# Kernel optimization log

Measured on AMD Instinct MI355X. Metric: run time of the kernel, lower is better.

The kernel has to match this reference:

```python
import jax, jax.numpy as jnp
import numpy as np

WS = 8          # window size
SS = WS // 2    # shift size
HEADS = 16
DIM = 512
H = W = 256
L = WS * WS


def _rel_pos_index(ws):
    coords = np.stack(np.meshgrid(np.arange(ws), np.arange(ws), indexing='ij')).reshape(2, -1)
    rel = coords[:, :, None] - coords[:, None, :]            # (2, L, L)
    return (rel[0] + ws - 1) * (2 * ws - 1) + (rel[1] + ws - 1)  # (L, L)


def _shift_mask(H, W, ws, ss):
    m = np.zeros((H, W), np.int32)
    cnt = 0
    for hs in (slice(0, -ws), slice(-ws, -ss), slice(-ss, None)):
        for wsl in (slice(0, -ws), slice(-ws, -ss), slice(-ss, None)):
            m[hs, wsl] = cnt
            cnt += 1
    m = m.reshape(H // ws, ws, W // ws, ws).transpose(0, 2, 1, 3).reshape(-1, ws * ws)
    return m[:, None, :] != m[:, :, None]  # (num_windows, L, L) bool


REL_IDX = jnp.asarray(_rel_pos_index(WS))          # (L, L) int32
MASK = jnp.asarray(_shift_mask(H, W, WS, SS))      # (nw, L, L) bool


def setup_inputs() -> dict:
    key = jax.random.key(0)
    ks = jax.random.split(key, 16)
    d = DIM
    s = lambda *sh: 1.0 / np.sqrt(sh[0])
    return {
        'x': jax.random.normal(ks[0], (1, d, H, W), jnp.float32),
        'norm1_w': jnp.ones((d,), jnp.float32),
        'norm1_b': jnp.zeros((d,), jnp.float32),
        'qkv_w': jax.random.normal(ks[1], (d, 3 * d), jnp.float32) * s(d),
        'qkv_b': jnp.zeros((3 * d,), jnp.float32),
        'proj_w': jax.random.normal(ks[2], (d, d), jnp.float32) * s(d),
        'proj_b': jnp.zeros((d,), jnp.float32),
        'rel_bias_table': jax.random.normal(ks[3], ((2 * WS - 1) ** 2, HEADS), jnp.float32) * 0.02,
        'gamma1': jnp.full((d,), 1e-6, jnp.float32),
        'norm2_w': jnp.ones((d,), jnp.float32),
        'norm2_b': jnp.zeros((d,), jnp.float32),
        'fc1_w': jax.random.normal(ks[4], (d, 4 * d), jnp.float32) * s(d),
        'fc1_b': jnp.zeros((4 * d,), jnp.float32),
        'fc2_w': jax.random.normal(ks[5], (4 * d, d), jnp.float32) * s(4 * d),
        'fc2_b': jnp.zeros((d,), jnp.float32),
        'gamma2': jnp.full((d,), 1e-6, jnp.float32),
    }


def _ln(z, w, b, eps=1e-5):
    mu = z.mean(-1, keepdims=True)
    var = ((z - mu) ** 2).mean(-1, keepdims=True)
    return (z - mu) * jax.lax.rsqrt(var + eps) * w + b


def reference(x, norm1_w, norm1_b, qkv_w, qkv_b, proj_w, proj_b, rel_bias_table,
              gamma1, norm2_w, norm2_b, fc1_w, fc1_b, fc2_w, fc2_b, gamma2):
    B, C, Hh, Ww = x.shape
    hd = C // HEADS
    # cyclic shift
    xs = jnp.roll(x, (-SS, -SS), axis=(2, 3))
    # window partition: (B,C,H,W) -> (B*nw, L, C)
    win = xs.reshape(B, C, Hh // WS, WS, Ww // WS, WS)
    win = win.transpose(0, 2, 4, 3, 5, 1).reshape(-1, L, C)
    nw = win.shape[0]

    xn = _ln(win, norm1_w, norm1_b)
    qkv = xn @ qkv_w + qkv_b                                  # (nw, L, 3C)
    q, k, v = jnp.split(qkv, 3, axis=-1)
    q = q.reshape(nw, L, HEADS, hd).transpose(0, 2, 1, 3)
    k = k.reshape(nw, L, HEADS, hd).transpose(0, 2, 1, 3)
    v = v.reshape(nw, L, HEADS, hd).transpose(0, 2, 1, 3)

    attn = jnp.einsum('whld,whmd->whlm', q, k) * (hd ** -0.5)  # (nw,heads,L,L)
    rel_bias = rel_bias_table[REL_IDX].transpose(2, 0, 1)      # (heads, L, L)
    attn = attn + rel_bias[None]
    attn = jnp.where(MASK[:, None], -jnp.inf, attn)            # shift mask
    a = jax.nn.softmax(attn, axis=-1)
    out = jnp.einsum('whlm,whmd->whld', a, v)
    out = out.transpose(0, 2, 1, 3).reshape(nw, L, C)
    out = out @ proj_w + proj_b

    o1 = win + gamma1 * out
    h = jax.nn.gelu(_ln(o1, norm2_w, norm2_b) @ fc1_w + fc1_b, approximate=False)
    o2 = o1 + gamma2 * (h @ fc2_w + fc2_b)

    # window reverse: (nw, L, C) -> (B, C, H, W)
    o2 = o2.reshape(B, Hh // WS, Ww // WS, WS, WS, C)
    o2 = o2.transpose(0, 5, 1, 3, 2, 4).reshape(B, C, Hh, Ww)
    return jnp.roll(o2, (SS, SS), axis=(2, 3))
```

## Files before the change

kernel.cpp:

```cpp
#include <hip/hip_runtime.h>
#include <cstdint>


typedef __bf16 bf16x8 __attribute__((ext_vector_type(8)));
typedef float f32x4 __attribute__((ext_vector_type(4)));
typedef unsigned short ushortx4 __attribute__((ext_vector_type(4)));
typedef unsigned short ushortx8 __attribute__((ext_vector_type(8)));
typedef unsigned short u16;

__device__ __forceinline__ float b2f(u16 u) {
  union { unsigned u32; float f; } c; c.u32 = ((unsigned)u) << 16; return c.f;
}
__device__ __forceinline__ u16 f2b(float f) {
  union { float f; unsigned u; } c; c.f = f;
  unsigned r = c.u + 0x7FFFu + ((c.u >> 16) & 1u);
  return (u16)(r >> 16);
}

__device__ __forceinline__ void async_ld16(const void* g, void* l) {
  __builtin_amdgcn_global_load_lds(
      (__attribute__((address_space(1))) void*)(g),
      (__attribute__((address_space(3))) void*)(l), 16, 0, 0);
}

__device__ __forceinline__ int tok2sp(int t) {
  const int hs = ((t >> 11) << 3) | ((t >> 3) & 7);
  const int wsb = (((t >> 6) & 31) << 3) | (t & 7);
  return ((hs + 4) & 255) * 256 + ((wsb + 4) & 255);
}

#define C_N1W 0
#define C_N1B 512
#define C_N2W 1024
#define C_N2B 1536
#define C_G1 2048
#define C_G2 2560
#define C_PROJB 3072
#define C_FC2B 3584
#define C_QKVB 4096
#define C_FC1B 5632
#define C_RELB 7680

__global__ void detect_k(const u16* n1w, int* flag) {
  if (threadIdx.x == 0 && blockIdx.x == 0)
    *flag = (n1w[0] != 0x3F80u) ? 1 : 0;
}

__device__ __forceinline__ void conv(const void* s, u16* d, int n, int flag,
                                     int tid) {
  if (flag) {
    const float* f = (const float*)s;
    for (int i = tid; i < n; i += 256) d[i] = f2b(f[i]);
  } else {
    const u16* u = (const u16*)s;
    for (int i = tid; i < n; i += 256) d[i] = u[i];
  }
}

__global__ __launch_bounds__(256) void canon_k(
    const void* n1w, const void* n1b, const void* n2w, const void* n2b,
    const void* g1, const void* g2, const void* pb, const void* f2bv,
    const void* qb, const void* f1b, const void* rb, u16* canon,
    const int* flagp) {
  const int flag = *flagp;
  const int tid = threadIdx.x;
  conv(n1w, canon + C_N1W, 512, flag, tid);
  conv(n1b, canon + C_N1B, 512, flag, tid);
  conv(n2w, canon + C_N2W, 512, flag, tid);
  conv(n2b, canon + C_N2B, 512, flag, tid);
  conv(g1, canon + C_G1, 512, flag, tid);
  conv(g2, canon + C_G2, 512, flag, tid);
  conv(pb, canon + C_PROJB, 512, flag, tid);
  conv(f2bv, canon + C_FC2B, 512, flag, tid);
  conv(qb, canon + C_QKVB, 1536, flag, tid);
  conv(f1b, canon + C_FC1B, 2048, flag, tid);
  conv(rb, canon + C_RELB, 3600, flag, tid);
}

__global__ __launch_bounds__(256) void packw_k(
    const void* __restrict__ W, u16* __restrict__ dst, int K, int N,
    const int* __restrict__ flagp) {
  const int flag = *flagp;
  const int K32 = K >> 5;
  const long base = ((long)blockIdx.x * 256 + threadIdx.x) * 16;
#pragma unroll
  for (int g = 0; g < 2; ++g) {
    const long i0 = base + g * 8;
    const int w = (int)(i0 & 4095);
    const int n_ = (w >> 3) & 127;
    const int rg = w >> 10;
    const long tile = i0 >> 12;
    const int kt = (int)(tile % K32);
    const int panel = (int)(tile / K32);
    const int n = panel * 128 + n_;
    const int kb = kt * 32 + rg * 8;
    ushortx8 out;
#pragma unroll
    for (int r7 = 0; r7 < 8; ++r7) {
      const long src = (long)(kb + r7) * N + n;
      out[r7] = flag ? f2b(((const float*)W)[src]) : ((const u16*)W)[src];
    }
    *(ushortx8*)(dst + i0) = out;
  }
}

__global__ __launch_bounds__(256) void ln1_win_k(
    const void* __restrict__ x, const u16* __restrict__ canon,
    u16* __restrict__ xn, int t0, const int* __restrict__ flagp) {
  const int flag = *flagp;
  const int tid = threadIdx.x;
  const int q = tid >> 4;
  const int cb = tid & 15;
  const int row = q >> 1, half = q & 1;

  const int win = (t0 >> 6) + blockIdx.x;
  const int wh = win >> 5, ww = win & 31;
  const int hr = ((wh << 3) + 4 + row) & 255;
  const int wc = ((ww << 3) + 4 + (half << 2)) & 255;
  const long sp4 = (long)hr * 256 + wc;

  __shared__ float red[2][16][17][4];
  __shared__ float mu_s[64], rs_s[64];
  __shared__ u16 wb[1024];
  __shared__ __align__(16) u16 tbuf[64 * 280];

  for (int i = tid; i < 1024; i += 256) wb[i] = canon[i];

  f32x4 dat[32];
  if (flag) {
    const float* xf = (const float*)x + sp4 + (long)cb * 65536;
#pragma unroll
    for (int it = 0; it < 32; ++it)
      dat[it] = *(const f32x4*)(xf + (long)it * (16 * 65536));
  } else {
    const u16* xu = (const u16*)x + sp4 + (long)cb * 65536;
#pragma unroll
    for (int it = 0; it < 32; ++it) {
      const ushortx4 v = *(const ushortx4*)(xu + (long)it * (16 * 65536));
#pragma unroll
      for (int j = 0; j < 4; ++j) dat[it][j] = b2f(v[j]);
    }
  }

  float sum[4] = {0.f, 0.f, 0.f, 0.f}, sq[4] = {0.f, 0.f, 0.f, 0.f};
#pragma unroll
  for (int it = 0; it < 32; ++it)
#pragma unroll
    for (int j = 0; j < 4; ++j) {
      sum[j] += dat[it][j];
      sq[j] += dat[it][j] * dat[it][j];
    }
#pragma unroll
  for (int j = 0; j < 4; ++j) {
    red[0][cb][q][j] = sum[j];
    red[1][cb][q][j] = sq[j];
  }
  __syncthreads();
  if (tid < 64) {
    const int rt = tid >> 3, ct = tid & 7;
    const int qt = rt * 2 + (ct >> 2), jt = ct & 3;
    float s = 0.f, s2 = 0.f;
#pragma unroll
    for (int b = 0; b < 16; ++b) {
      s += red[0][b][qt][jt];
      s2 += red[1][b][qt][jt];
    }
    const float mu = s * (1.f / 512.f);
    mu_s[tid] = mu;
    rs_s[tid] = rsqrtf(fmaxf(s2 * (1.f / 512.f) - mu * mu, 0.f) + 1e-5f);
  }
  __syncthreads();

  float mur[4], rsr[4];
#pragma unroll
  for (int j = 0; j < 4; ++j) {
    const int t = (row << 3) + (half << 2) + j;
    mur[j] = mu_s[t];
    rsr[j] = rs_s[t];
  }

#pragma unroll
  for (int h = 0; h < 2; ++h) {
#pragma unroll
    for (int ih = 0; ih < 16; ++ih) {
      const int it = h * 16 + ih;
      const int c = cb + (it << 4);
      const float wv = b2f(wb[c]);
      const float bv = b2f(wb[512 + c]);
      const int cof = c & 255;
#pragma unroll
      for (int j = 0; j < 4; ++j) {
        const int t = (row << 3) + (half << 2) + j;
        tbuf[t * 280 + cof] = f2b((dat[it][j] - mur[j]) * rsr[j] * wv + bv);
      }
    }
    __syncthreads();
    {
      const int to = tid >> 2, cg = tid & 3;
      u16* dst = xn + ((long)(blockIdx.x * 64 + to) * 512) + (h << 8);
#pragma unroll
      for (int it2 = 0; it2 < 8; ++it2) {
        const int ch = cg + (it2 << 2);
        *(ushortx8*)(dst + ch * 8) = *(const ushortx8*)&tbuf[to * 280 + ch * 8];
      }
    }
    __syncthreads();
  }
}

__global__ __launch_bounds__(256) void ln2_k(
    const u16* __restrict__ src, const u16* __restrict__ canon,
    u16* __restrict__ dst) {
  const int wave = threadIdx.x >> 6, lane = threadIdx.x & 63;
  const int t = blockIdx.x * 4 + wave;
  const u16* row = src + (long)t * 512 + lane * 8;
  ushortx4 v0 = *(const ushortx4*)row;
  ushortx4 v1 = *(const ushortx4*)(row + 4);
  float f[8];
#pragma unroll
  for (int j = 0; j < 4; ++j) { f[j] = b2f(v0[j]); f[4 + j] = b2f(v1[j]); }
  float sum = 0.f, sq = 0.f;
#pragma unroll
  for (int j = 0; j < 8; ++j) { sum += f[j]; sq += f[j] * f[j]; }
#pragma unroll
  for (int off = 1; off < 64; off <<= 1) {
    sum += __shfl_xor(sum, off);
    sq += __shfl_xor(sq, off);
  }
  const float mu = sum * (1.f / 512.f);
  const float rsd = rsqrtf(fmaxf(sq * (1.f / 512.f) - mu * mu, 0.f) + 1e-5f);
  const int c0 = lane * 8;
  ushortx4 o0, o1v;
#pragma unroll
  for (int j = 0; j < 4; ++j) {
    o0[j] = f2b((f[j] - mu) * rsd * b2f(canon[C_N2W + c0 + j]) +
                b2f(canon[C_N2B + c0 + j]));
    o1v[j] = f2b((f[4 + j] - mu) * rsd * b2f(canon[C_N2W + c0 + 4 + j]) +
                 b2f(canon[C_N2B + c0 + 4 + j]));
  }
  u16* d = dst + (long)t * 512 + c0;
  *(ushortx4*)d = o0;
  *(ushortx4*)(d + 4) = o1v;
}

template <int EPI>
__global__ __launch_bounds__(256) void gemm_bt(
    const u16* __restrict__ A, const u16* __restrict__ Wp,
    const u16* __restrict__ bias, void* __restrict__ Cv, int N, int K,
    const void* __restrict__ aux, const u16* __restrict__ gamma, int t0,
    const int* flagp) {
  __shared__ __align__(16) u16 lsA[4096];
  __shared__ __align__(16) u16 lsB[4096];
  const int flag = *flagp;
  const int tid = threadIdx.x;
  const int wave = tid >> 6;
  const int lane = tid & 63;
  const int bm = blockIdx.y << 7;
  const int bn = blockIdx.x << 7;
  const int wm = (wave >> 1) << 6;
  const int wn = (wave & 1) << 6;
  const int K32 = K >> 5;
  u16* C = (u16*)Cv;

  f32x4 acc[4][4] = {};

  const int u0 = (wave * 2) * 64 + lane;
  const int u1 = u0 + 64;
  const int r0 = u0 & 127, k0g = (u0 >> 7) * 8;
  const int r1 = u1 & 127, k1g = (u1 >> 7) * 8;
  const u16* a0 = A + (long)(bm + r0) * K + k0g;
  const u16* a1 = A + (long)(bm + r1) * K + k1g;
  u16* la0 = &lsA[(wave * 2 + 0) * 512];
  u16* la1 = &lsA[(wave * 2 + 1) * 512];

  const u16* wp0 = Wp + (long)(bn >> 7) * K32 * 4096 + (wave * 2 + 0) * 512 +
                   lane * 8;
  const u16* wp1 = wp0 + 512;
  u16* lb0 = &lsB[(wave * 2 + 0) * 512];
  u16* lb1 = &lsB[(wave * 2 + 1) * 512];

  const int fr = lane & 15;
  const int kg = lane >> 4;

  for (int kk = 0; kk < K; kk += 32) {
    __syncthreads();
    async_ld16(a0 + kk, la0);
    async_ld16(a1 + kk, la1);
    async_ld16(wp0 + (long)(kk >> 5) * 4096, lb0);
    async_ld16(wp1 + (long)(kk >> 5) * 4096, lb1);
    __syncthreads();
    bf16x8 af[4], bfr[4];
#pragma unroll
    for (int i = 0; i < 4; ++i)
      af[i] = *(const bf16x8*)&lsA[(kg * 128 + wm + i * 16 + fr) * 8];
#pragma unroll
    for (int j = 0; j < 4; ++j)
      bfr[j] = *(const bf16x8*)&lsB[(kg * 128 + wn + j * 16 + fr) * 8];
#pragma unroll
    for (int i = 0; i < 4; ++i)
#pragma unroll
      for (int j = 0; j < 4; ++j)
        acc[i][j] =
            __builtin_amdgcn_mfma_f32_16x16x32_bf16(af[i], bfr[j], acc[i][j], 0, 0, 0);
  }

  const int cl = lane & 15;
  const int rq = (lane >> 4) << 2;
  float bv[4], gv[4];
#pragma unroll
  for (int j = 0; j < 4; ++j) {
    const int col = bn + wn + j * 16 + cl;
    bv[j] = b2f(bias[col]);
    gv[j] = (EPI == 1 || EPI == 3) ? b2f(gamma[col]) : 0.f;
  }
#pragma unroll
  for (int i = 0; i < 4; ++i) {
    const int tbase = bm + wm + i * 16 + rq;
    long spb = 0;
    if (EPI == 1 || EPI == 3) spb = tok2sp(t0 + tbase);
#pragma unroll
    for (int j = 0; j < 4; ++j) {
      const int col = bn + wn + j * 16 + cl;
      if (EPI == 0) {
#pragma unroll
        for (int p = 0; p < 4; ++p)
          C[(long)(tbase + p) * N + col] = f2b(acc[i][j][p] + bv[j]);
      } else if (EPI == 2) {
#pragma unroll
        for (int p = 0; p < 4; ++p) {
          float v = acc[i][j][p] + bv[j];
          C[(long)(tbase + p) * N + col] =
              f2b(0.5f * v * (1.0f + erff(v * 0.70710678118654752f)));
        }
      } else if (EPI == 1) {
        float xg[4];
        if (flag) {
          const f32x4 x4 = *(const f32x4*)((const float*)aux + (long)col * 65536 + spb);
#pragma unroll
          for (int p = 0; p < 4; ++p) xg[p] = x4[p];
        } else {
          const ushortx4 x4 = *(const ushortx4*)((const u16*)aux + (long)col * 65536 + spb);
#pragma unroll
          for (int p = 0; p < 4; ++p) xg[p] = b2f(x4[p]);
        }
#pragma unroll
        for (int p = 0; p < 4; ++p) {
          float corr = gv[j] * (acc[i][j][p] + bv[j]);
          corr = fminf(fmaxf(corr, -0.01f), 0.01f);
          C[(long)(tbase + p) * N + col] = f2b(xg[p] + corr);
        }
      } else {
        float ov[4];
#pragma unroll
        for (int p = 0; p < 4; ++p) {
          float corr = gv[j] * (acc[i][j][p] + bv[j]);
          corr = fminf(fmaxf(corr, -0.01f), 0.01f);
          ov[p] = b2f(((const u16*)aux)[(long)(tbase + p) * 512 + col]) + corr;
        }
        if (flag) {
          f32x4 o4;
#pragma unroll
          for (int p = 0; p < 4; ++p) o4[p] = ov[p];
          *(f32x4*)&((float*)Cv)[(long)col * 65536 + spb] = o4;
        } else {
          ushortx4 o4;
#pragma unroll
          for (int p = 0; p < 4; ++p) o4[p] = f2b(ov[p]);
          *(ushortx4*)&((u16*)Cv)[(long)col * 65536 + spb] = o4;
        }
      }
    }
  }
}

__global__ __launch_bounds__(256) void attn_k(
    const u16* __restrict__ qkv, const u16* __restrict__ canon,
    u16* __restrict__ out, int win0) {
  const int tid = threadIdx.x;
  const int wave = tid >> 6, lane = tid & 63;
  const int winl = blockIdx.x >> 2;
  const int head = ((blockIdx.x & 3) << 2) + wave;
  const int wing = winl + win0;
  const int wh = wing >> 5, ww = wing & 31;
  const int g = lane >> 4, a = lane & 15;

  __shared__ __align__(16) u16 alds[28672];
  u16* P  = alds + wave * 7168;
  u16* VT = P + 4608;
  u16* HB = VT + 2304;

  for (int i5 = lane; i5 < 225; i5 += 64)
    HB[i5] = canon[C_RELB + i5 * 16 + head];

  const long tb = (long)winl * 64;
  const u16* q_base = qkv + tb * 1536 + head * 32;

  {
    const u16* vrow = q_base + 1024 + (long)lane * 1536;
    const ushortx8 v0 = *(const ushortx8*)(vrow);
    const ushortx8 v1 = *(const ushortx8*)(vrow + 8);
    const ushortx8 v2 = *(const ushortx8*)(vrow + 16);
    const ushortx8 v3 = *(const ushortx8*)(vrow + 24);
#pragma unroll
    for (int d2 = 0; d2 < 8; ++d2) {
      VT[(d2 +  0) * 72 + (lane ^ (( d2       & 7) << 3))] = v0[d2];
      VT[(d2 +  8) * 72 + (lane ^ (((d2 +  8) & 7) << 3))] = v1[d2];
      VT[(d2 + 16) * 72 + (lane ^ (((d2 + 16) & 7) << 3))] = v2[d2];
      VT[(d2 + 24) * 72 + (lane ^ (((d2 + 24) & 7) << 3))] = v3[d2];
    }
  }

  f32x4 acc[4][4] = {};
  {
    bf16x8 af[4], bf[4];
#pragma unroll
    for (int i = 0; i < 4; ++i)
      af[i] = *(const bf16x8*)(q_base + (long)(i * 16 + a) * 1536 + g * 8);
#pragma unroll
    for (int j = 0; j < 4; ++j)
      bf[j] = *(const bf16x8*)(q_base + 512 + (long)(j * 16 + a) * 1536 + g * 8);
#pragma unroll
    for (int i = 0; i < 4; ++i)
#pragma unroll
      for (int j = 0; j < 4; ++j)
        acc[i][j] = __builtin_amdgcn_mfma_f32_16x16x32_bf16(af[i], bf[j],
                                                            acc[i][j], 0, 0, 0);
  }

  const float SCALE = 0.17677669529663687f;
  const int whE = (wh == 31), wwE = (ww == 31);
  const int RW = wwE ? ((lane >> 4) & 1) + 1 : 0;
  const int CW = wwE ? ((lane >> 2) & 1) + 1 : 0;
#pragma unroll
  for (int i = 0; i < 4; ++i) {
    const int RH = whE ? (i >> 1) + 1 : 0;
#pragma unroll
    for (int j = 0; j < 4; ++j) {
      const int CH = whE ? (j >> 1) + 1 : 0;
      const bool msk = (RH * 3 + RW) != (CH * 3 + CW);
      const int base = (i * 2 + (lane >> 5) - j * 2 - ((lane >> 3) & 1) + 7) * 15
                       + (g & 1) * 4 - (a & 7) + 7;
#pragma unroll
      for (int p = 0; p < 4; ++p) {
        const float s = acc[i][j][p] * SCALE + b2f(HB[base + p]);
        acc[i][j][p] = msk ? -1e30f : s;
      }
    }
  }

#pragma unroll
  for (int i = 0; i < 4; ++i) {
#pragma unroll
    for (int p = 0; p < 4; ++p) {
      float m = fmaxf(fmaxf(acc[i][0][p], acc[i][1][p]),
                      fmaxf(acc[i][2][p], acc[i][3][p]));
      m = fmaxf(m, __shfl_xor(m, 1));
      m = fmaxf(m, __shfl_xor(m, 2));
      m = fmaxf(m, __shfl_xor(m, 4));
      m = fmaxf(m, __shfl_xor(m, 8));
      float sum = 0.f;
#pragma unroll
      for (int j = 0; j < 4; ++j) {
        const float e = __expf(acc[i][j][p] - m);
        acc[i][j][p] = e;
        sum += e;
      }
      sum += __shfl_xor(sum, 1);
      sum += __shfl_xor(sum, 2);
      sum += __shfl_xor(sum, 4);
      sum += __shfl_xor(sum, 8);
      const float inv = 1.0f / sum;
#pragma unroll
      for (int j = 0; j < 4; ++j) acc[i][j][p] *= inv;
    }
  }

#pragma unroll
  for (int i = 0; i < 4; ++i) {
#pragma unroll
    for (int p = 0; p < 4; ++p) {
      const int q = i * 16 + g * 4 + p;
      u16* prow = P + q * 72;
      const int swz = (q & 7) << 3;
#pragma unroll
      for (int j = 0; j < 4; ++j)
        prow[(j * 16 + a) ^ swz] = f2b(acc[i][j][p]);
    }
  }

  f32x4 oacc[4][2] = {};
#pragma unroll
  for (int ks = 0; ks < 2; ++ks) {
    bf16x8 pa[4], vb[2];
#pragma unroll
    for (int i = 0; i < 4; ++i) {
      const int q = i * 16 + a;
      pa[i] = *(const bf16x8*)&P[q * 72 + ((ks * 32 + g * 8) ^ ((q & 7) << 3))];
    }
#pragma unroll
    for (int j2 = 0; j2 < 2; ++j2) {
      const int n = j2 * 16 + a;
      vb[j2] = *(const bf16x8*)&VT[n * 72 + ((ks * 32 + g * 8) ^ ((n & 7) << 3))];
    }
#pragma unroll
    for (int i = 0; i < 4; ++i)
#pragma unroll
      for (int j2 = 0; j2 < 2; ++j2)
        oacc[i][j2] = __builtin_amdgcn_mfma_f32_16x16x32_bf16(pa[i], vb[j2],
                                                              oacc[i][j2], 0, 0, 0);
  }

  u16* orow = out + tb * 512 + head * 32;
#pragma unroll
  for (int i = 0; i < 4; ++i)
#pragma unroll
    for (int p = 0; p < 4; ++p) {
      const int q = i * 16 + g * 4 + p;
#pragma unroll
      for (int j2 = 0; j2 < 2; ++j2)
        orow[(long)q * 512 + j2 * 16 + a] = f2b(oacc[i][j2][p]);
    }
}

extern "C" void kernel_launch(void* const* d_in, const int* in_sizes, int n_in,
                              void* d_out, int out_size, void* d_ws, size_t ws_size,
                              hipStream_t stream) {
  (void)in_sizes; (void)n_in; (void)out_size;
  const void* x = d_in[0];

  char* ws = (char*)d_ws;
  int* flagp = (int*)ws;
  u16* canon = (u16*)(ws + 4096);

  u16* wpack = (u16*)(ws + 65536);
  u16* wp_qkv = wpack;
  u16* wp_proj = wpack + 786432;
  u16* wp_fc1 = wpack + 1048576;
  u16* wp_fc2 = wpack + 2097152;
  const long CHUNK_BASE = 65536 + 6815744;

  long T = 256;
  for (long cand = 16384; cand >= 256; cand >>= 1) {
    if (CHUNK_BASE + cand * 10240 <= (long)ws_size) { T = cand; break; }
  }
  u16* xn   = (u16*)(ws + CHUNK_BASE);
  u16* qkvb = xn + T * 512;
  u16* o1   = qkvb + T * 1536;
  u16* l2b  = o1 + T * 512;
  u16* hb   = l2b + T * 512;
  u16* attn = xn;

  detect_k<<<1, 64, 0, stream>>>((const u16*)d_in[1], flagp);
  canon_k<<<1, 256, 0, stream>>>(d_in[1], d_in[2], d_in[9], d_in[10], d_in[8],
                                 d_in[15], d_in[6], d_in[14], d_in[4], d_in[12],
                                 d_in[7], canon, flagp);
  packw_k<<<192, 256, 0, stream>>>(d_in[3], wp_qkv, 512, 1536, flagp);
  packw_k<<<64, 256, 0, stream>>>(d_in[5], wp_proj, 512, 512, flagp);
  packw_k<<<256, 256, 0, stream>>>(d_in[11], wp_fc1, 512, 2048, flagp);
  packw_k<<<256, 256, 0, stream>>>(d_in[13], wp_fc2, 2048, 512, flagp);

  const int nchunk = (int)(65536 / T);
  for (int c = 0; c < nchunk; ++c) {
    const int t0 = (int)(c * T);
    ln1_win_k<<<(int)(T / 64), 256, 0, stream>>>(x, canon, xn, t0, flagp);
    gemm_bt<0><<<dim3(12, (int)(T / 128)), 256, 0, stream>>>(
        xn, wp_qkv, canon + C_QKVB, qkvb, 1536, 512, nullptr, nullptr, 0, flagp);
    attn_k<<<(int)(T / 64) * 4, 256, 0, stream>>>(qkvb, canon, attn, t0 / 64);
    gemm_bt<1><<<dim3(4, (int)(T / 128)), 256, 0, stream>>>(
        attn, wp_proj, canon + C_PROJB, o1, 512, 512, x, canon + C_G1, t0, flagp);
    ln2_k<<<(int)(T / 4), 256, 0, stream>>>(o1, canon, l2b);
    gemm_bt<2><<<dim3(16, (int)(T / 128)), 256, 0, stream>>>(
        l2b, wp_fc1, canon + C_FC1B, hb, 2048, 512, nullptr, nullptr, 0, flagp);
    gemm_bt<3><<<dim3(4, (int)(T / 128)), 256, 0, stream>>>(
        hb, wp_fc2, canon + C_FC2B, d_out, 512, 2048, o1, canon + C_G2, t0, flagp);
  }
}
```

Before: 1.449 ms.

## Double-buffer GEMM LDS loads, swizzle workgroup order, use fast erf in GELU

Turns the GEMM main loop into a double-buffered pipeline: the async global-to-LDS loads for the next K-step are issued before computing on the current buffer, with explicit vmcnt waits and barriers. Also remaps workgroup IDs with an 8-way swizzle to improve cache locality, and replaces erff in the GELU epilogue with an Abramowitz-Stegun polynomial approximation. LDS use doubles, and the erf approximation adds small error (around 1e-7 absolute).

```diff
diff --git a/kernel.cpp b/kernel.cpp
--- a/kernel.cpp
+++ b/kernel.cpp
@@ -21,6 +21,17 @@
   __builtin_amdgcn_global_load_lds(
       (__attribute__((address_space(1))) void*)(g),
       (__attribute__((address_space(3))) void*)(l), 16, 0, 0);
+}
+
+__device__ __forceinline__ float erf_fast(float x) {
+  const float ax = fabsf(x);
+  const float t = 1.0f / fmaf(0.3275911f, ax, 1.0f);
+  float p = fmaf(1.061405429f, t, -1.453152027f);
+  p = fmaf(p, t, 1.421413741f);
+  p = fmaf(p, t, -0.284496736f);
+  p = fmaf(p, t, 0.254829592f);
+  const float r = 1.0f - p * t * __expf(-ax * ax);
+  return copysignf(r, x);
 }
 
 __device__ __forceinline__ int tok2sp(int t) {
@@ -249,14 +260,20 @@
     const u16* __restrict__ bias, void* __restrict__ Cv, int N, int K,
     const void* __restrict__ aux, const u16* __restrict__ gamma, int t0,
     const int* flagp) {
-  __shared__ __align__(16) u16 lsA[4096];
-  __shared__ __align__(16) u16 lsB[4096];
+  __shared__ __align__(16) u16 lsA[2][4096];
+  __shared__ __align__(16) u16 lsB[2][4096];
   const int flag = *flagp;
   const int tid = threadIdx.x;
   const int wave = tid >> 6;
   const int lane = tid & 63;
-  const int bm = blockIdx.y << 7;
-  const int bn = blockIdx.x << 7;
+
+  const int gx = gridDim.x;
+  const int nwg = gx * gridDim.y;
+  const int wg0 = blockIdx.y * gx + blockIdx.x;
+  const int swz = (wg0 & 7) * (nwg >> 3) + (wg0 >> 3);
+  const int bn = (swz % gx) << 7;
+  const int bm = (swz / gx) << 7;
+
   const int wm = (wave >> 1) << 6;
   const int wn = (wave & 1) << 6;
   const int K32 = K >> 5;
@@ -270,38 +287,53 @@
   const int r1 = u1 & 127, k1g = (u1 >> 7) * 8;
   const u16* a0 = A + (long)(bm + r0) * K + k0g;
   const u16* a1 = A + (long)(bm + r1) * K + k1g;
-  u16* la0 = &lsA[(wave * 2 + 0) * 512];
-  u16* la1 = &lsA[(wave * 2 + 1) * 512];
-
   const u16* wp0 = Wp + (long)(bn >> 7) * K32 * 4096 + (wave * 2 + 0) * 512 +
                    lane * 8;
   const u16* wp1 = wp0 + 512;
-  u16* lb0 = &lsB[(wave * 2 + 0) * 512];
-  u16* lb1 = &lsB[(wave * 2 + 1) * 512];
+  const int c0 = (wave * 2 + 0) * 512;
+  const int c1 = (wave * 2 + 1) * 512;
 
   const int fr = lane & 15;
   const int kg = lane >> 4;
 
+  async_ld16(a0, &lsA[0][c0]);
+  async_ld16(a1, &lsA[0][c1]);
+  async_ld16(wp0, &lsB[0][c0]);
+  async_ld16(wp1, &lsB[0][c1]);
+
+  int cur = 0;
   for (int kk = 0; kk < K; kk += 32) {
-    __syncthreads();
-    async_ld16(a0 + kk, la0);
-    async_ld16(a1 + kk, la1);
-    async_ld16(wp0 + (long)(kk >> 5) * 4096, lb0);
-    async_ld16(wp1 + (long)(kk >> 5) * 4096, lb1);
-    __syncthreads();
+    if (kk + 32 < K) {
+      const int nb = cur ^ 1;
+      async_ld16(a0 + kk + 32, &lsA[nb][c0]);
+      async_ld16(a1 + kk + 32, &lsA[nb][c1]);
+      async_ld16(wp0 + (long)((kk >> 5) + 1) * 4096, &lsB[nb][c0]);
+      async_ld16(wp1 + (long)((kk >> 5) + 1) * 4096, &lsB[nb][c1]);
+      __builtin_amdgcn_sched_barrier(0);
+      asm volatile("s_waitcnt vmcnt(4)" ::: "memory");
+    } else {
+      asm volatile("s_waitcnt vmcnt(0)" ::: "memory");
+    }
+    __builtin_amdgcn_sched_barrier(0);
+    __builtin_amdgcn_s_barrier();
+    __builtin_amdgcn_sched_barrier(0);
     bf16x8 af[4], bfr[4];
 #pragma unroll
     for (int i = 0; i < 4; ++i)
-      af[i] = *(const bf16x8*)&lsA[(kg * 128 + wm + i * 16 + fr) * 8];
+      af[i] = *(const bf16x8*)&lsA[cur][(kg * 128 + wm + i * 16 + fr) * 8];
 #pragma unroll
     for (int j = 0; j < 4; ++j)
-      bfr[j] = *(const bf16x8*)&lsB[(kg * 128 + wn + j * 16 + fr) * 8];
+      bfr[j] = *(const bf16x8*)&lsB[cur][(kg * 128 + wn + j * 16 + fr) * 8];
 #pragma unroll
     for (int i = 0; i < 4; ++i)
 #pragma unroll
       for (int j = 0; j < 4; ++j)
         acc[i][j] =
             __builtin_amdgcn_mfma_f32_16x16x32_bf16(af[i], bfr[j], acc[i][j], 0, 0, 0);
+    __builtin_amdgcn_sched_barrier(0);
+    __builtin_amdgcn_s_barrier();
+    __builtin_amdgcn_sched_barrier(0);
+    cur ^= 1;
   }
 
   const int cl = lane & 15;
@@ -330,7 +362,7 @@
         for (int p = 0; p < 4; ++p) {
           float v = acc[i][j][p] + bv[j];
           C[(long)(tbase + p) * N + col] =
-              f2b(0.5f * v * (1.0f + erff(v * 0.70710678118654752f)));
+              f2b(0.5f * v * (1.0f + erf_fast(v * 0.70710678118654752f)));
         }
       } else if (EPI == 1) {
         float xg[4];
```

Measured after the change: 1.291 ms. 10.9% less time.
